# Performance work log

Measured on AMD Instinct MI355X. Metric: run time of the kernel, lower is better.

Reference implementation:

```python
import jax, jax.numpy as jnp
import numpy as np

D_MODEL = 768
D_INNER = 1536   # expand=2
D_STATE = 16
D_CONV = 4
DT_RANK = 48     # ceil(768/16)
B_SZ, L = 2, 2048


def _mamba(h, in_proj, conv_w, conv_b, xproj, dtproj_w, dtproj_b, A_log, Dskip, out_proj):
    """One Mamba block forward. h: [B, L, d_model]."""
    B = h.shape[0]
    xz = h @ in_proj.T                      # [B, L, 2*d_inner]
    x, z = jnp.split(xz, 2, axis=-1)
    # causal depthwise conv over time
    xc = jnp.transpose(x, (0, 2, 1))        # [B, D, L]
    xc = jax.lax.conv_general_dilated(
        xc, conv_w[:, None, :], (1,), [(D_CONV - 1, 0)],
        dimension_numbers=('NCH', 'OIH', 'NCH'), feature_group_count=D_INNER)
    xc = xc + conv_b[None, :, None]
    x = jax.nn.silu(jnp.transpose(xc, (0, 2, 1)))   # [B, L, D]
    # input-dependent dt, B, C
    dbl = x @ xproj.T                                # [B, L, dt_rank + 2*d_state]
    dt, Bm, Cm = jnp.split(dbl, [DT_RANK, DT_RANK + D_STATE], axis=-1)
    dt = jax.nn.softplus(dt @ dtproj_w.T + dtproj_b) # [B, L, D]
    A = -jnp.exp(A_log)                              # [D, N]

    def step(hst, inp):
        x_t, dt_t, B_t, C_t = inp                    # [B,D],[B,D],[B,N],[B,N]
        dA = jnp.exp(dt_t[..., None] * A)            # [B, D, N]
        hst = hst * dA + dt_t[..., None] * B_t[:, None, :] * x_t[..., None]
        y = jnp.einsum('bdn,bn->bd', hst, C_t)
        return hst, y

    h0 = jnp.zeros((B, D_INNER, D_STATE), dtype=h.dtype)
    xs = (jnp.transpose(x, (1, 0, 2)), jnp.transpose(dt, (1, 0, 2)),
          jnp.transpose(Bm, (1, 0, 2)), jnp.transpose(Cm, (1, 0, 2)))
    _, ys = jax.lax.scan(step, h0, xs)               # ys: [L, B, D]
    y = jnp.transpose(ys, (1, 0, 2)) + x * Dskip
    y = y * jax.nn.silu(z)
    return y @ out_proj.T                            # [B, L, d_model]


def _init_params(key):
    ks = jax.random.split(key, 7)
    s = 0.02
    in_proj = jax.random.normal(ks[0], (2 * D_INNER, D_MODEL)) * s
    conv_w = jax.random.normal(ks[1], (D_INNER, D_CONV)) * 0.2
    conv_b = jnp.zeros((D_INNER,))
    xproj = jax.random.normal(ks[2], (DT_RANK + 2 * D_STATE, D_INNER)) * s
    dtproj_w = jax.random.normal(ks[3], (D_INNER, DT_RANK)) * (DT_RANK ** -0.5)
    dtproj_b = jnp.log(jax.random.uniform(ks[4], (D_INNER,), minval=1e-3, maxval=0.1))
    A_log = jnp.log(jnp.tile(jnp.arange(1, D_STATE + 1, dtype=jnp.float32), (D_INNER, 1)))
    Dskip = jnp.ones((D_INNER,))
    out_proj = jax.random.normal(ks[5], (D_MODEL, D_INNER)) * s
    return in_proj, conv_w, conv_b, xproj, dtproj_w, dtproj_b, A_log, Dskip, out_proj


def setup_inputs() -> dict:
    key = jax.random.key(0)
    k_h, k_f, k_r = jax.random.split(key, 3)
    inp = {'hidden_states': jax.random.normal(k_h, (B_SZ, L, D_MODEL), dtype=jnp.float32)}
    names = ['in_proj', 'conv_w', 'conv_b', 'xproj', 'dtproj_w', 'dtproj_b', 'A_log', 'Dskip', 'out_proj']
    for suf, k in (('_f', k_f), ('_r', k_r)):
        for n, p in zip(names, _init_params(k)):
            inp[n + suf] = p
    return inp


def reference(hidden_states,
              in_proj_f, conv_w_f, conv_b_f, xproj_f, dtproj_w_f, dtproj_b_f, A_log_f, Dskip_f, out_proj_f,
              in_proj_r, conv_w_r, conv_b_r, xproj_r, dtproj_w_r, dtproj_b_r, A_log_r, Dskip_r, out_proj_r):
    out = _mamba(hidden_states, in_proj_f, conv_w_f, conv_b_f, xproj_f,
                 dtproj_w_f, dtproj_b_f, A_log_f, Dskip_f, out_proj_f)
    out_rev = _mamba(hidden_states[:, ::-1, :], in_proj_r, conv_w_r, conv_b_r, xproj_r,
                     dtproj_w_r, dtproj_b_r, A_log_r, Dskip_r, out_proj_r)[:, ::-1, :]
    return out + out_rev
```

## Files before the change

kernel.cpp:

```cpp
#include <hip/hip_runtime.h>
#include <hip/hip_bf16.h>
#include <math.h>

#define L_SEQ 2048
#define B_SZ 2
#define D_MODEL 768
#define D_INNER 1536
#define D_STATE 16
#define DT_RANK 48
#define TC 64
#define NC (L_SEQ / TC)
#define NDG (D_INNER / 256)
#define NSPL 4
#define KCH (D_INNER / NSPL)

typedef short bf16x8 __attribute__((ext_vector_type(8)));
typedef float f32x4 __attribute__((ext_vector_type(4)));

#define GLOAD16(g, l) __builtin_amdgcn_global_load_lds( \
    (const __attribute__((address_space(1))) unsigned*)(g), \
    (__attribute__((address_space(3))) unsigned*)(l), 16, 0, 0)

static __device__ __forceinline__ float siluf(float v) {
  return v / (1.0f + __expf(-v));
}
static __device__ __forceinline__ float softplusf(float v) {
  return fmaxf(v, 0.0f) + log1pf(__expf(-fabsf(v)));
}
static __device__ __forceinline__ unsigned short f2bf_rn(float v) {
  unsigned u = __float_as_uint(v);
  u = (u + 0x7fff + ((u >> 16) & 1)) >> 16;
  return (unsigned short)u;
}
static __device__ __forceinline__ float bf2f(unsigned short v) {
  return __uint_as_float((unsigned)v << 16);
}

__global__ __launch_bounds__(256) void cvt_all(
    const float* __restrict__ s_h,  unsigned short* __restrict__ hh,  unsigned short* __restrict__ hl,
    const float* __restrict__ s_w0, unsigned short* __restrict__ w0h, unsigned short* __restrict__ w0l,
    const float* __restrict__ s_w1, unsigned short* __restrict__ w1h, unsigned short* __restrict__ w1l,
    const float* __restrict__ s_o0, unsigned short* __restrict__ o0h, unsigned short* __restrict__ o0l,
    const float* __restrict__ s_o1, unsigned short* __restrict__ o1h, unsigned short* __restrict__ o1l,
    const float* __restrict__ s_x0, unsigned short* __restrict__ x0h, unsigned short* __restrict__ x0l,
    const float* __restrict__ s_x1, unsigned short* __restrict__ x1h, unsigned short* __restrict__ x1l)
{
  long j = (long)blockIdx.x * 256 + threadIdx.x;
  const long N0 = 786432, N1 = 589824, N2 = 589824, N3 = 294912, N4 = 294912, N5 = 30720;
  const float* src; unsigned short *dh, *dl;
  if (j < N0) { src = s_h; dh = hh; dl = hl; }
  else if ((j -= N0) < N1) { src = s_w0; dh = w0h; dl = w0l; }
  else if ((j -= N1) < N2) { src = s_w1; dh = w1h; dl = w1l; }
  else if ((j -= N2) < N3) { src = s_o0; dh = o0h; dl = o0l; }
  else if ((j -= N3) < N4) { src = s_o1; dh = o1h; dl = o1l; }
  else if ((j -= N4) < N5) { src = s_x0; dh = x0h; dl = x0l; }
  else { j -= N5; src = s_x1; dh = x1h; dl = x1l; }
  float4 v = ((const float4*)src)[j];
  float vv[4] = {v.x, v.y, v.z, v.w};
  unsigned short h4[4], l4[4];
  #pragma unroll
  for (int e = 0; e < 4; ++e) {
    unsigned short hv = f2bf_rn(vv[e]);
    h4[e] = hv;
    l4[e] = f2bf_rn(vv[e] - bf2f(hv));
  }
  uint2 ph, pl;
  ph.x = (unsigned)h4[0] | ((unsigned)h4[1] << 16);
  ph.y = (unsigned)h4[2] | ((unsigned)h4[3] << 16);
  pl.x = (unsigned)l4[0] | ((unsigned)l4[1] << 16);
  pl.y = (unsigned)l4[2] | ((unsigned)l4[3] << 16);
  *(uint2*)&dh[j * 4] = ph;
  *(uint2*)&dl[j * 4] = pl;
}

__global__ __launch_bounds__(256) void gemm_inproj(
    const unsigned short* __restrict__ hh, const unsigned short* __restrict__ hl,
    const unsigned short* __restrict__ w0h, const unsigned short* __restrict__ w0l,
    const unsigned short* __restrict__ w1h, const unsigned short* __restrict__ w1l,
    float* __restrict__ xpre, float* __restrict__ zbuf)
{
  __shared__ unsigned short Ah[128 * 32], Al[128 * 32];
  __shared__ unsigned short Wh[128 * 32], Wl[128 * 32];
  const long S1 = (long)B_SZ * L_SEQ * D_INNER;
  const int tid = threadIdx.x;
  const int lane = tid & 63, w = tid >> 6;
  int bid = blockIdx.x;
  int swz = (bid & 7) * 192 + (bid >> 3);
  int dir = swz / 768;
  int rem = swz - dir * 768;
  int mb = rem / 24, nb = rem - (rem / 24) * 24;
  const int m0 = mb * 128, n0 = nb * 128;
  const unsigned short* Whp = dir ? w1h : w0h;
  const unsigned short* Wlp = dir ? w1l : w0l;
  const int ksl = (lane & 3) ^ ((lane >> 3) & 3);
  long aoff[2], woff[2];
  int ldsc[2];
  #pragma unroll
  for (int qq = 0; qq < 2; ++qq) {
    int cq = w * 2 + qq;
    int r = cq * 16 + (lane >> 2);
    int mr = m0 + r;
    int row = dir ? ((mr & ~(L_SEQ - 1)) | ((L_SEQ - 1) - (mr & (L_SEQ - 1)))) : mr;
    aoff[qq] = (long)row * D_MODEL + 8 * ksl;
    woff[qq] = (long)(n0 + r) * D_MODEL + 8 * ksl;
    ldsc[qq] = cq * 512;
  }
  f32x4 acc[4][4];
  #pragma unroll
  for (int i = 0; i < 4; ++i)
    #pragma unroll
    for (int j = 0; j < 4; ++j) acc[i][j] = (f32x4){0.f, 0.f, 0.f, 0.f};
  const int fr = lane & 15, sl = lane >> 4;
  const int wr = w >> 1, wc = w & 1;
  int roffA[4], roffW[4];
  #pragma unroll
  for (int f = 0; f < 4; ++f) {
    int rA = wr * 64 + f * 16 + fr;
    roffA[f] = rA * 32 + ((sl ^ ((rA >> 1) & 3)) * 8);
    int rW = wc * 64 + f * 16 + fr;
    roffW[f] = rW * 32 + ((sl ^ ((rW >> 1) & 3)) * 8);
  }
  for (int k0 = 0; k0 < D_MODEL; k0 += 32) {
    __syncthreads();
    #pragma unroll
    for (int qq = 0; qq < 2; ++qq) {
      GLOAD16(hh + aoff[qq] + k0, &Ah[ldsc[qq]]);
      GLOAD16(hl + aoff[qq] + k0, &Al[ldsc[qq]]);
      GLOAD16(Whp + woff[qq] + k0, &Wh[ldsc[qq]]);
      GLOAD16(Wlp + woff[qq] + k0, &Wl[ldsc[qq]]);
    }
    __syncthreads();
    bf16x8 afh[4], afl[4];
    #pragma unroll
    for (int f = 0; f < 4; ++f) {
      afh[f] = *(const bf16x8*)&Ah[roffA[f]];
      afl[f] = *(const bf16x8*)&Al[roffA[f]];
    }
    #pragma unroll
    for (int fj = 0; fj < 4; ++fj) {
      bf16x8 wfh = *(const bf16x8*)&Wh[roffW[fj]];
      bf16x8 wfl = *(const bf16x8*)&Wl[roffW[fj]];
      #pragma unroll
      for (int fi = 0; fi < 4; ++fi) {
        acc[fi][fj] = __builtin_amdgcn_mfma_f32_16x16x32_bf16(afh[fi], wfh, acc[fi][fj], 0, 0, 0);
        acc[fi][fj] = __builtin_amdgcn_mfma_f32_16x16x32_bf16(afh[fi], wfl, acc[fi][fj], 0, 0, 0);
        acc[fi][fj] = __builtin_amdgcn_mfma_f32_16x16x32_bf16(afl[fi], wfh, acc[fi][fj], 0, 0, 0);
      }
    }
  }
  float* xq = xpre + (long)dir * S1;
  float* zq = zbuf + (long)dir * S1;
  const int fcol = lane & 15, rgrp = lane >> 4;
  #pragma unroll
  for (int fi = 0; fi < 4; ++fi) {
    #pragma unroll
    for (int j = 0; j < 4; ++j) {
      int row = m0 + wr * 64 + fi * 16 + rgrp * 4 + j;
      #pragma unroll
      for (int fj = 0; fj < 4; ++fj) {
        int n = n0 + wc * 64 + fj * 16 + fcol;
        float v = acc[fi][fj][j];
        if (n < D_INNER) xq[(long)row * D_INNER + n] = v;
        else             zq[(long)row * D_INNER + (n - D_INNER)] = v;
      }
    }
  }
}

__global__ __launch_bounds__(256) void xproj_mfma(
    const unsigned short* __restrict__ xh, const unsigned short* __restrict__ xl,
    const unsigned short* __restrict__ x0h, const unsigned short* __restrict__ x0l,
    const unsigned short* __restrict__ x1h, const unsigned short* __restrict__ x1l,
    float* __restrict__ partial)
{
  __shared__ unsigned short Ah[128 * 32], Al[128 * 32];
  __shared__ unsigned short Wh[128 * 32], Wl[128 * 32];
  const long S1 = (long)B_SZ * L_SEQ * D_INNER;
  const int tid = threadIdx.x;
  const int lane = tid & 63, w = tid >> 6;
  int bid = blockIdx.x;
  int dir = bid >> 7;
  int kz = (bid >> 5) & 3;
  int mb = bid & 31;
  const int m0 = mb * 128;
  const int kbase = kz * KCH;
  const unsigned short* Ahp = xh + (long)dir * S1;
  const unsigned short* Alp = xl + (long)dir * S1;
  const unsigned short* Whp = dir ? x1h : x0h;
  const unsigned short* Wlp = dir ? x1l : x0l;
  const int ksl = (lane & 3) ^ ((lane >> 3) & 3);
  long aoff[2], woff[2];
  int ldsc[2], cqv[2];
  #pragma unroll
  for (int qq = 0; qq < 2; ++qq) {
    int cq = w * 2 + qq;
    int r = cq * 16 + (lane >> 2);
    aoff[qq] = (long)(m0 + r) * D_INNER + 8 * ksl + kbase;
    woff[qq] = (long)r * D_INNER + 8 * ksl + kbase;
    ldsc[qq] = cq * 512;
    cqv[qq] = cq;
  }
  for (int i = tid; i < 48 * 32; i += 256) { Wh[80 * 32 + i] = 0; Wl[80 * 32 + i] = 0; }
  f32x4 acc[4][4];
  #pragma unroll
  for (int i = 0; i < 4; ++i)
    #pragma unroll
    for (int j = 0; j < 4; ++j) acc[i][j] = (f32x4){0.f, 0.f, 0.f, 0.f};
  const int fr = lane & 15, sl = lane >> 4;
  const int wr = w >> 1, wc = w & 1;
  int roffA[4], roffW[4];
  #pragma unroll
  for (int f = 0; f < 4; ++f) {
    int rA = wr * 64 + f * 16 + fr;
    roffA[f] = rA * 32 + ((sl ^ ((rA >> 1) & 3)) * 8);
    int rW = wc * 64 + f * 16 + fr;
    roffW[f] = rW * 32 + ((sl ^ ((rW >> 1) & 3)) * 8);
  }
  for (int k0 = 0; k0 < KCH; k0 += 32) {
    __syncthreads();
    #pragma unroll
    for (int qq = 0; qq < 2; ++qq) {
      GLOAD16(Ahp + aoff[qq] + k0, &Ah[ldsc[qq]]);
      GLOAD16(Alp + aoff[qq] + k0, &Al[ldsc[qq]]);
      if (cqv[qq] < 5) {
        GLOAD16(Whp + woff[qq] + k0, &Wh[ldsc[qq]]);
        GLOAD16(Wlp + woff[qq] + k0, &Wl[ldsc[qq]]);
      }
    }
    __syncthreads();
    bf16x8 afh[4], afl[4];
    #pragma unroll
    for (int f = 0; f < 4; ++f) {
      afh[f] = *(const bf16x8*)&Ah[roffA[f]];
      afl[f] = *(const bf16x8*)&Al[roffA[f]];
    }
    #pragma unroll
    for (int fj = 0; fj < 4; ++fj) {
      bf16x8 wfh = *(const bf16x8*)&Wh[roffW[fj]];
      bf16x8 wfl = *(const bf16x8*)&Wl[roffW[fj]];
      #pragma unroll
      for (int fi = 0; fi < 4; ++fi) {
        acc[fi][fj] = __builtin_amdgcn_mfma_f32_16x16x32_bf16(afh[fi], wfh, acc[fi][fj], 0, 0, 0);
        acc[fi][fj] = __builtin_amdgcn_mfma_f32_16x16x32_bf16(afh[fi], wfl, acc[fi][fj], 0, 0, 0);
        acc[fi][fj] = __builtin_amdgcn_mfma_f32_16x16x32_bf16(afl[fi], wfh, acc[fi][fj], 0, 0, 0);
      }
    }
  }
  float* P = partial + (long)(dir * NSPL + kz) * (B_SZ * L_SEQ) * 80;
  const int fcol = lane & 15, rgrp = lane >> 4;
  #pragma unroll
  for (int fi = 0; fi < 4; ++fi) {
    #pragma unroll
    for (int j = 0; j < 4; ++j) {
      int row = m0 + wr * 64 + fi * 16 + rgrp * 4 + j;
      #pragma unroll
      for (int fj = 0; fj < 4; ++fj) {
        int n = wc * 64 + fj * 16 + fcol;
        if (n < 80) P[(long)row * 80 + n] = acc[fi][fj][j];
      }
    }
  }
}

__global__ __launch_bounds__(256) void xproj_reduce(
    const float* __restrict__ partial, float* __restrict__ dbl)
{
  long idx = (long)blockIdx.x * 256 + threadIdx.x;
  const long plane = (long)B_SZ * L_SEQ * 80;
  long dir = idx / plane;
  long rc = idx % plane;
  const float* P = partial + dir * NSPL * plane + rc;
  float s = 0.f;
  #pragma unroll
  for (int z = 0; z < NSPL; ++z) s += P[z * plane];
  dbl[idx] = s;
}

__global__ __launch_bounds__(256) void gemm_outproj_pl(
    const unsigned short* __restrict__ yh, const unsigned short* __restrict__ yl,
    const unsigned short* __restrict__ o0h, const unsigned short* __restrict__ o0l,
    const unsigned short* __restrict__ o1h, const unsigned short* __restrict__ o1l,
    float* __restrict__ partial)
{
  __shared__ unsigned short Ah[128 * 32], Al[128 * 32];
  __shared__ unsigned short Wh[128 * 32], Wl[128 * 32];
  const long S1 = (long)B_SZ * L_SEQ * D_INNER;
  const int tid = threadIdx.x;
  const int lane = tid & 63, w = tid >> 6;
  int bid = blockIdx.x;
  int swz = (bid & 7) * 96 + (bid >> 3);
  int dir = swz / 384;
  int r1 = swz - dir * 384;
  int ks = r1 / 192;
  int r2 = r1 - ks * 192;
  int mb = r2 / 6, nb = r2 - (r2 / 6) * 6;
  const int m0 = mb * 128, n0 = nb * 128;
  const int kbase = ks * (D_INNER / 2);
  const unsigned short* Ahp = yh + (long)dir * S1;
  const unsigned short* Alp = yl + (long)dir * S1;
  const unsigned short* Whp = dir ? o1h : o0h;
  const unsigned short* Wlp = dir ? o1l : o0l;
  const int ksl = (lane & 3) ^ ((lane >> 3) & 3);
  long aoff[2], woff[2];
  int ldsc[2];
  #pragma unroll
  for (int qq = 0; qq < 2; ++qq) {
    int cq = w * 2 + qq;
    int r = cq * 16 + (lane >> 2);
    int mr = m0 + r;
    int row = dir ? ((mr & ~(L_SEQ - 1)) | ((L_SEQ - 1) - (mr & (L_SEQ - 1)))) : mr;
    aoff[qq] = (long)row * D_INNER + 8 * ksl + kbase;
    woff[qq] = (long)(n0 + r) * D_INNER + 8 * ksl + kbase;
    ldsc[qq] = cq * 512;
  }
  f32x4 acc[4][4];
  #pragma unroll
  for (int i = 0; i < 4; ++i)
    #pragma unroll
    for (int j = 0; j < 4; ++j) acc[i][j] = (f32x4){0.f, 0.f, 0.f, 0.f};
  const int fr = lane & 15, sl = lane >> 4;
  const int wr = w >> 1, wc = w & 1;
  int roffA[4], roffW[4];
  #pragma unroll
  for (int f = 0; f < 4; ++f) {
    int rA = wr * 64 + f * 16 + fr;
    roffA[f] = rA * 32 + ((sl ^ ((rA >> 1) & 3)) * 8);
    int rW = wc * 64 + f * 16 + fr;
    roffW[f] = rW * 32 + ((sl ^ ((rW >> 1) & 3)) * 8);
  }
  for (int k0 = 0; k0 < D_INNER / 2; k0 += 32) {
    __syncthreads();
    #pragma unroll
    for (int qq = 0; qq < 2; ++qq) {
      GLOAD16(Ahp + aoff[qq] + k0, &Ah[ldsc[qq]]);
      GLOAD16(Alp + aoff[qq] + k0, &Al[ldsc[qq]]);
      GLOAD16(Whp + woff[qq] + k0, &Wh[ldsc[qq]]);
      GLOAD16(Wlp + woff[qq] + k0, &Wl[ldsc[qq]]);
    }
    __syncthreads();
    bf16x8 afh[4], afl[4];
    #pragma unroll
    for (int f = 0; f < 4; ++f) {
      afh[f] = *(const bf16x8*)&Ah[roffA[f]];
      afl[f] = *(const bf16x8*)&Al[roffA[f]];
    }
    #pragma unroll
    for (int fj = 0; fj < 4; ++fj) {
      bf16x8 wfh = *(const bf16x8*)&Wh[roffW[fj]];
      bf16x8 wfl = *(const bf16x8*)&Wl[roffW[fj]];
      #pragma unroll
      for (int fi = 0; fi < 4; ++fi) {
        acc[fi][fj] = __builtin_amdgcn_mfma_f32_16x16x32_bf16(afh[fi], wfh, acc[fi][fj], 0, 0, 0);
        acc[fi][fj] = __builtin_amdgcn_mfma_f32_16x16x32_bf16(afh[fi], wfl, acc[fi][fj], 0, 0, 0);
        acc[fi][fj] = __builtin_amdgcn_mfma_f32_16x16x32_bf16(afl[fi], wfh, acc[fi][fj], 0, 0, 0);
      }
    }
  }
  float* P = partial + (long)(dir * 2 + ks) * (B_SZ * L_SEQ) * D_MODEL;
  const int fcol = lane & 15, rgrp = lane >> 4;
  #pragma unroll
  for (int fi = 0; fi < 4; ++fi) {
    #pragma unroll
    for (int j = 0; j < 4; ++j) {
      int row = m0 + wr * 64 + fi * 16 + rgrp * 4 + j;
      #pragma unroll
      for (int fj = 0; fj < 4; ++fj) {
        int n = n0 + wc * 64 + fj * 16 + fcol;
        P[(long)row * D_MODEL + n] = acc[fi][fj][j];
      }
    }
  }
}

__global__ __launch_bounds__(256) void outproj_reduce(
    const float* __restrict__ partial, float* __restrict__ out)
{
  long i = (long)blockIdx.x * 256 + threadIdx.x;
  const long plane4 = (long)B_SZ * L_SEQ * D_MODEL / 4;
  float4 a = ((const float4*)partial)[i];
  float4 b = ((const float4*)partial)[i + plane4];
  float4 c = ((const float4*)partial)[i + 2 * plane4];
  float4 d = ((const float4*)partial)[i + 3 * plane4];
  float4 s;
  s.x = (a.x + b.x) + (c.x + d.x);
  s.y = (a.y + b.y) + (c.y + d.y);
  s.z = (a.z + b.z) + (c.z + d.z);
  s.w = (a.w + b.w) + (c.w + d.w);
  ((float4*)out)[i] = s;
}

__global__ __launch_bounds__(256) void conv_silu_pl(
    const float* __restrict__ xpre,
    const float* __restrict__ w_f, const float* __restrict__ b_f,
    const float* __restrict__ w_r, const float* __restrict__ b_r,
    unsigned short* __restrict__ xh, unsigned short* __restrict__ xl)
{
  long i4 = (long)blockIdx.x * 256 + threadIdx.x;
  const long total4 = 2L * B_SZ * L_SEQ * D_INNER / 4;
  if (i4 >= total4) return;
  long idx = i4 * 4;
  int d0 = (int)(idx % D_INNER);
  long r = idx / D_INNER;
  int t = (int)(r & (L_SEQ - 1));
  const float* w  = (r >> 12) ? w_r : w_f;
  const float* cb = (r >> 12) ? b_r : b_f;
  float4 a = *(const float4*)&cb[d0];
  float4 wc[4];
  #pragma unroll
  for (int i = 0; i < 4; ++i) wc[i] = *(const float4*)&w[(d0 + i) * 4];
  #pragma unroll
  for (int k = 0; k < 4; ++k) {
    if (t - 3 + k >= 0) {
      float4 xv = *(const float4*)&xpre[(r - 3 + k) * D_INNER + d0];
      a.x = fmaf(((const float*)&wc[0])[k], xv.x, a.x);
      a.y = fmaf(((const float*)&wc[1])[k], xv.y, a.y);
      a.z = fmaf(((const float*)&wc[2])[k], xv.z, a.z);
      a.w = fmaf(((const float*)&wc[3])[k], xv.w, a.w);
    }
  }
  float vv[4] = {siluf(a.x), siluf(a.y), siluf(a.z), siluf(a.w)};
  unsigned short h4[4], l4[4];
  #pragma unroll
  for (int e = 0; e < 4; ++e) {
    unsigned short hv = f2bf_rn(vv[e]);
    h4[e] = hv;
    l4[e] = f2bf_rn(vv[e] - bf2f(hv));
  }
  uint2 ph, pl;
  ph.x = (unsigned)h4[0] | ((unsigned)h4[1] << 16);
  ph.y = (unsigned)h4[2] | ((unsigned)h4[3] << 16);
  pl.x = (unsigned)l4[0] | ((unsigned)l4[1] << 16);
  pl.y = (unsigned)l4[2] | ((unsigned)l4[3] << 16);
  *(uint2*)&xh[idx] = ph;
  *(uint2*)&xl[idx] = pl;
}

__global__ __launch_bounds__(256) void scan_mega1(
    const unsigned short* __restrict__ xh, const unsigned short* __restrict__ xl,
    const float* __restrict__ dbl,
    const float* __restrict__ dtw_f, const float* __restrict__ dtw_r,
    const float* __restrict__ dtb_f, const float* __restrict__ dtb_r,
    const float* __restrict__ A_log_f, const float* __restrict__ A_log_r,
    float* __restrict__ stateS, float* __restrict__ stateP)
{
  const int tid = threadIdx.x;
  const int chunk = blockIdx.x / NDG;
  const int d = (blockIdx.x % NDG) * 256 + tid;
  const int b = blockIdx.y, dir = blockIdx.z;
  const float* A_log = dir ? A_log_r : A_log_f;
  const float* dtw   = dir ? dtw_r : dtw_f;
  const float dtbv   = (dir ? dtb_r : dtb_f)[d];
  float wreg[48];
  #pragma unroll
  for (int q = 0; q < 12; ++q)
    *(float4*)&wreg[q * 4] = *(const float4*)&dtw[d * DT_RANK + q * 4];
  float Arow[D_STATE];
  #pragma unroll
  for (int n = 0; n < D_STATE; ++n) Arow[n] = -expf(A_log[d * D_STATE + n]);
  float h[D_STATE], P[D_STATE];
  #pragma unroll
  for (int n = 0; n < D_STATE; ++n) { h[n] = 0.f; P[n] = 1.f; }
  const long rowbase = ((long)dir * B_SZ + b) * L_SEQ + (long)chunk * TC;
  for (int tj = 0; tj < TC; ++tj) {
    const float* br = dbl + (rowbase + tj) * 80;
    float dtacc = 0.f;
    #pragma unroll
    for (int q = 0; q < 12; ++q) {
      float4 v = *(const float4*)(br + q * 4);
      dtacc = fmaf(v.x, wreg[q * 4 + 0], dtacc);
      dtacc = fmaf(v.y, wreg[q * 4 + 1], dtacc);
      dtacc = fmaf(v.z, wreg[q * 4 + 2], dtacc);
      dtacc = fmaf(v.w, wreg[q * 4 + 3], dtacc);
    }
    float dtv = softplusf(dtacc + dtbv);
    long off = (rowbase + tj) * D_INNER + d;
    float xv = bf2f(xh[off]) + bf2f(xl[off]);
    float dtx = dtv * xv;
    float bc[D_STATE];
    #pragma unroll
    for (int q = 0; q < 4; ++q)
      *(float4*)&bc[q * 4] = *(const float4*)(br + 48 + q * 4);
    #pragma unroll
    for (int n = 0; n < D_STATE; ++n) {
      float dA = __expf(dtv * Arow[n]);
      P[n] *= dA;
      h[n] = fmaf(h[n], dA, dtx * bc[n]);
    }
  }
  long base = ((((long)dir * B_SZ + b) * NC + chunk) * D_INNER + d) * D_STATE;
  #pragma unroll
  for (int n = 0; n < D_STATE; ++n) { stateS[base + n] = h[n]; stateP[base + n] = P[n]; }
}

__global__ __launch_bounds__(256) void scan_fix(
    float* __restrict__ stateS, const float* __restrict__ stateP)
{
  const long idx = (long)blockIdx.x * 256 + threadIdx.x;
  const int DN = D_INNER * D_STATE;
  const long dirb = idx / DN;
  const int dn = (int)(idx % DN);
  long base = dirb * NC * DN + dn;
  float h = 0.f;
  for (int c = 0; c < NC; ++c) {
    long o = base + (long)c * DN;
    float S = stateS[o];
    float Pc = stateP[o];
    stateS[o] = h;
    h = fmaf(h, Pc, S);
  }
}

__global__ __launch_bounds__(256) void scan_mega2(
    const unsigned short* __restrict__ xh, const unsigned short* __restrict__ xl,
    const float* __restrict__ dbl, const float* __restrict__ z,
    const float* __restrict__ dtw_f, const float* __restrict__ dtw_r,
    const float* __restrict__ dtb_f, const float* __restrict__ dtb_r,
    const float* __restrict__ A_log_f, const float* __restrict__ A_log_r,
    const float* __restrict__ Ds_f, const float* __restrict__ Ds_r,
    const float* __restrict__ stateS,
    unsigned short* __restrict__ yh, unsigned short* __restrict__ yl)
{
  const int tid = threadIdx.x;
  const int chunk = blockIdx.x / NDG;
  const int d = (blockIdx.x % NDG) * 256 + tid;
  const int b = blockIdx.y, dir = blockIdx.z;
  const float* A_log = dir ? A_log_r : A_log_f;
  const float* dtw   = dir ? dtw_r : dtw_f;
  const float dtbv   = (dir ? dtb_r : dtb_f)[d];
  const float Dd     = (dir ? Ds_r : Ds_f)[d];
  float wreg[48];
  #pragma unroll
  for (int q = 0; q < 12; ++q)
    *(float4*)&wreg[q * 4] = *(const float4*)&dtw[d * DT_RANK + q * 4];
  float Arow[D_STATE];
  #pragma unroll
  for (int n = 0; n < D_STATE; ++n) Arow[n] = -expf(A_log[d * D_STATE + n]);
  float h[D_STATE];
  long sbase = ((((long)dir * B_SZ + b) * NC + chunk) * D_INNER + d) * D_STATE;
  #pragma unroll
  for (int n = 0; n < D_STATE; ++n) h[n] = stateS[sbase + n];
  const long rowbase = ((long)dir * B_SZ + b) * L_SEQ + (long)chunk * TC;
  for (int tj = 0; tj < TC; ++tj) {
    const float* br = dbl + (rowbase + tj) * 80;
    float dtacc = 0.f;
    #pragma unroll
    for (int q = 0; q < 12; ++q) {
      float4 v = *(const float4*)(br + q * 4);
      dtacc = fmaf(v.x, wreg[q * 4 + 0], dtacc);
      dtacc = fmaf(v.y, wreg[q * 4 + 1], dtacc);
      dtacc = fmaf(v.z, wreg[q * 4 + 2], dtacc);
      dtacc = fmaf(v.w, wreg[q * 4 + 3], dtacc);
    }
    float dtv = softplusf(dtacc + dtbv);
    long off = (rowbase + tj) * D_INNER + d;
    float xv = bf2f(xh[off]) + bf2f(xl[off]);
    float zv = z[off];
    float dtx = dtv * xv;
    float bc[2 * D_STATE];
    #pragma unroll
    for (int q = 0; q < 8; ++q)
      *(float4*)&bc[q * 4] = *(const float4*)(br + 48 + q * 4);
    float y = 0.f;
    #pragma unroll
    for (int n = 0; n < D_STATE; ++n) {
      float dA = __expf(dtv * Arow[n]);
      h[n] = fmaf(h[n], dA, dtx * bc[n]);
      y = fmaf(h[n], bc[16 + n], y);
    }
    y = fmaf(xv, Dd, y);
    y *= siluf(zv);
    unsigned short hv = f2bf_rn(y);
    yh[off] = hv;
    yl[off] = f2bf_rn(y - bf2f(hv));
  }
}

extern "C" void kernel_launch(void* const* d_in, const int* in_sizes, int n_in,
                              void* d_out, int out_size, void* d_ws, size_t ws_size,
                              hipStream_t stream) {
  const float* h        = (const float*)d_in[0];
  const float* in_proj[2] = {(const float*)d_in[1], (const float*)d_in[10]};
  const float* conv_w[2]  = {(const float*)d_in[2], (const float*)d_in[11]};
  const float* conv_b[2]  = {(const float*)d_in[3], (const float*)d_in[12]};
  const float* xproj[2]   = {(const float*)d_in[4], (const float*)d_in[13]};
  const float* dtw[2]     = {(const float*)d_in[5], (const float*)d_in[14]};
  const float* dtb[2]     = {(const float*)d_in[6], (const float*)d_in[15]};
  const float* A_log[2]   = {(const float*)d_in[7], (const float*)d_in[16]};
  const float* Dsk[2]     = {(const float*)d_in[8], (const float*)d_in[17]};
  const float* outp[2]    = {(const float*)d_in[9], (const float*)d_in[18]};
  float* out = (float*)d_out;
  float* ws = (float*)d_ws;

  const long S1 = (long)B_SZ * L_SEQ * D_INNER;
  const int M = B_SZ * L_SEQ;
  float* xpre  = ws;
  float* zbuf  = ws + 2 * S1;
  float* xconv = ws + 4 * S1;
  float* dbl   = ws + 6 * S1;
  float* base4 = dbl + 2L * M * 80;

  unsigned short* hh  = (unsigned short*)base4;
  unsigned short* hl  = hh + 3145728;
  unsigned short* w0h = hl + 3145728;
  unsigned short* w0l = w0h + 2359296;
  unsigned short* w1h = w0l + 2359296;
  unsigned short* w1l = w1h + 2359296;
  unsigned short* o0h = w1l + 2359296;
  unsigned short* o0l = o0h + 1179648;
  unsigned short* o1h = o0l + 1179648;
  unsigned short* o1l = o1h + 1179648;
  float* xpartial = base4;
  float* stS = base4;
  float* stP = stS + 3145728;
  unsigned short* xw0h = (unsigned short*)dbl;
  unsigned short* xw0l = xw0h + 122880;
  unsigned short* xw1h = xw0l + 122880;
  unsigned short* xw1l = xw1h + 122880;
  unsigned short* xph = (unsigned short*)xconv;
  unsigned short* xpl = xph + 2 * S1;
  unsigned short* yh = (unsigned short*)xpre;
  unsigned short* yl = yh + 2 * S1;
  float* opartial = xconv;

  dim3 blk(256);

  cvt_all<<<dim3(10224), blk, 0, stream>>>(
      h, hh, hl, in_proj[0], w0h, w0l, in_proj[1], w1h, w1l,
      outp[0], o0h, o0l, outp[1], o1h, o1l,
      xproj[0], xw0h, xw0l, xproj[1], xw1h, xw1l);

  gemm_inproj<<<dim3(1536), blk, 0, stream>>>(hh, hl, w0h, w0l, w1h, w1l, xpre, zbuf);

  conv_silu_pl<<<dim3((unsigned)(2 * S1 / 4 / 256)), blk, 0, stream>>>(
      xpre, conv_w[0], conv_b[0], conv_w[1], conv_b[1], xph, xpl);

  xproj_mfma<<<dim3(256), blk, 0, stream>>>(xph, xpl, xw0h, xw0l, xw1h, xw1l, xpartial);
  xproj_reduce<<<dim3((unsigned)(2L * M * 80 / 256)), blk, 0, stream>>>(xpartial, dbl);

  {
    dim3 grid1(NC * NDG, B_SZ, 2);
    scan_mega1<<<grid1, blk, 0, stream>>>(xph, xpl, dbl,
        dtw[0], dtw[1], dtb[0], dtb[1], A_log[0], A_log[1], stS, stP);
    long nfix = 2L * B_SZ * D_INNER * D_STATE;
    scan_fix<<<dim3((unsigned)(nfix / 256)), blk, 0, stream>>>(stS, stP);
    scan_mega2<<<grid1, blk, 0, stream>>>(xph, xpl, dbl, zbuf,
        dtw[0], dtw[1], dtb[0], dtb[1], A_log[0], A_log[1],
        Dsk[0], Dsk[1], stS, yh, yl);
  }
  gemm_outproj_pl<<<dim3(768), blk, 0, stream>>>(yh, yl, o0h, o0l, o1h, o1l, opartial);
  outproj_reduce<<<dim3((unsigned)(M * (long)D_MODEL / 4 / 256)), blk, 0, stream>>>(opartial, out);
}
```

Before: 493.6 us.

## Split dt dot into four accumulators, batch conv over 4 timesteps, prefetch scan_fix loads

The 48-wide dt projection dot product in both scan kernels now uses four independent accumulators, and the time loops are unrolled by 2 to shorten the FMA dependency chain. The depthwise conv kernel has each thread compute four consecutive timesteps from a 7-row window, so the overlapping input rows are read once instead of up to four times. scan_fix loads all chunk states into registers before the sequential combine, which takes the global loads off the serial path. The costs are higher register pressure in the scan kernels and in scan_fix (64 extra floats), and a small change in floating-point summation order.

```diff
diff --git a/kernel.cpp b/kernel.cpp
--- a/kernel.cpp
+++ b/kernel.cpp
@@ -34,6 +34,27 @@
 }
 static __device__ __forceinline__ float bf2f(unsigned short v) {
   return __uint_as_float((unsigned)v << 16);
+}
+static __device__ __forceinline__ float dtdot48(const float* __restrict__ br,
+                                                const float* __restrict__ wreg) {
+  float a0 = 0.f, a1 = 0.f, a2 = 0.f, a3 = 0.f;
+  #pragma unroll
+  for (int q = 0; q < 3; ++q) {
+    float4 v0 = *(const float4*)(br + q * 16 + 0);
+    float4 v1 = *(const float4*)(br + q * 16 + 4);
+    float4 v2 = *(const float4*)(br + q * 16 + 8);
+    float4 v3 = *(const float4*)(br + q * 16 + 12);
+    const float* w = wreg + q * 16;
+    a0 = fmaf(v0.x, w[0], a0);  a0 = fmaf(v0.y, w[1], a0);
+    a0 = fmaf(v0.z, w[2], a0);  a0 = fmaf(v0.w, w[3], a0);
+    a1 = fmaf(v1.x, w[4], a1);  a1 = fmaf(v1.y, w[5], a1);
+    a1 = fmaf(v1.z, w[6], a1);  a1 = fmaf(v1.w, w[7], a1);
+    a2 = fmaf(v2.x, w[8], a2);  a2 = fmaf(v2.y, w[9], a2);
+    a2 = fmaf(v2.z, w[10], a2); a2 = fmaf(v2.w, w[11], a2);
+    a3 = fmaf(v3.x, w[12], a3); a3 = fmaf(v3.y, w[13], a3);
+    a3 = fmaf(v3.z, w[14], a3); a3 = fmaf(v3.w, w[15], a3);
+  }
+  return (a0 + a1) + (a2 + a3);
 }
 
 __global__ __launch_bounds__(256) void cvt_all(
@@ -389,50 +410,63 @@
   ((float4*)out)[i] = s;
 }
 
-__global__ __launch_bounds__(256) void conv_silu_pl(
+__global__ __launch_bounds__(256) void conv_silu_pl4(
     const float* __restrict__ xpre,
     const float* __restrict__ w_f, const float* __restrict__ b_f,
     const float* __restrict__ w_r, const float* __restrict__ b_r,
     unsigned short* __restrict__ xh, unsigned short* __restrict__ xl)
 {
-  long i4 = (long)blockIdx.x * 256 + threadIdx.x;
-  const long total4 = 2L * B_SZ * L_SEQ * D_INNER / 4;
-  if (i4 >= total4) return;
-  long idx = i4 * 4;
-  int d0 = (int)(idx % D_INNER);
-  long r = idx / D_INNER;
-  int t = (int)(r & (L_SEQ - 1));
-  const float* w  = (r >> 12) ? w_r : w_f;
-  const float* cb = (r >> 12) ? b_r : b_f;
-  float4 a = *(const float4*)&cb[d0];
+  long i = (long)blockIdx.x * 256 + threadIdx.x;
+  const int DQ = D_INNER / 4;
+  const long total = 2L * B_SZ * (L_SEQ / 4) * DQ;
+  if (i >= total) return;
+  int dq = (int)(i % DQ);
+  long rq = i / DQ;
+  int t0 = (int)((rq & (L_SEQ / 4 - 1)) * 4);
+  long rbase = (rq >> 9) * L_SEQ;
+  int dir = (int)(rq >> 10);
+  int d0 = dq * 4;
+  const float* w  = dir ? w_r : w_f;
+  const float* cb = dir ? b_r : b_f;
+  float4 bias = *(const float4*)&cb[d0];
   float4 wc[4];
   #pragma unroll
-  for (int i = 0; i < 4; ++i) wc[i] = *(const float4*)&w[(d0 + i) * 4];
-  #pragma unroll
-  for (int k = 0; k < 4; ++k) {
-    if (t - 3 + k >= 0) {
-      float4 xv = *(const float4*)&xpre[(r - 3 + k) * D_INNER + d0];
+  for (int c = 0; c < 4; ++c) wc[c] = *(const float4*)&w[(d0 + c) * 4];
+  float4 xrow[7];
+  #pragma unroll
+  for (int j = 0; j < 7; ++j) {
+    int tv = t0 + j - 3;
+    if (tv >= 0) xrow[j] = *(const float4*)&xpre[(rbase + tv) * D_INNER + d0];
+    else xrow[j] = (float4){0.f, 0.f, 0.f, 0.f};
+  }
+  #pragma unroll
+  for (int u = 0; u < 4; ++u) {
+    float4 a = bias;
+    #pragma unroll
+    for (int k = 0; k < 4; ++k) {
+      float4 xv = xrow[u + k];
       a.x = fmaf(((const float*)&wc[0])[k], xv.x, a.x);
       a.y = fmaf(((const float*)&wc[1])[k], xv.y, a.y);
       a.z = fmaf(((const float*)&wc[2])[k], xv.z, a.z);
       a.w = fmaf(((const float*)&wc[3])[k], xv.w, a.w);
     }
-  }
-  float vv[4] = {siluf(a.x), siluf(a.y), siluf(a.z), siluf(a.w)};
-  unsigned short h4[4], l4[4];
-  #pragma unroll
-  for (int e = 0; e < 4; ++e) {
-    unsigned short hv = f2bf_rn(vv[e]);
-    h4[e] = hv;
-    l4[e] = f2bf_rn(vv[e] - bf2f(hv));
-  }
-  uint2 ph, pl;
-  ph.x = (unsigned)h4[0] | ((unsigned)h4[1] << 16);
-  ph.y = (unsigned)h4[2] | ((unsigned)h4[3] << 16);
-  pl.x = (unsigned)l4[0] | ((unsigned)l4[1] << 16);
-  pl.y = (unsigned)l4[2] | ((unsigned)l4[3] << 16);
-  *(uint2*)&xh[idx] = ph;
-  *(uint2*)&xl[idx] = pl;
+    float vv[4] = {siluf(a.x), siluf(a.y), siluf(a.z), siluf(a.w)};
+    unsigned short h4[4], l4[4];
+    #pragma unroll
+    for (int e = 0; e < 4; ++e) {
+      unsigned short hv = f2bf_rn(vv[e]);
+      h4[e] = hv;
+      l4[e] = f2bf_rn(vv[e] - bf2f(hv));
+    }
+    uint2 ph, pl;
+    ph.x = (unsigned)h4[0] | ((unsigned)h4[1] << 16);
+    ph.y = (unsigned)h4[2] | ((unsigned)h4[3] << 16);
+    pl.x = (unsigned)l4[0] | ((unsigned)l4[1] << 16);
+    pl.y = (unsigned)l4[2] | ((unsigned)l4[3] << 16);
+    long off = (rbase + t0 + u) * D_INNER + d0;
+    *(uint2*)&xh[off] = ph;
+    *(uint2*)&xl[off] = pl;
+  }
 }
 
 __global__ __launch_bounds__(256) void scan_mega1(
@@ -461,18 +495,10 @@
   #pragma unroll
   for (int n = 0; n < D_STATE; ++n) { h[n] = 0.f; P[n] = 1.f; }
   const long rowbase = ((long)dir * B_SZ + b) * L_SEQ + (long)chunk * TC;
+  #pragma unroll 2
   for (int tj = 0; tj < TC; ++tj) {
     const float* br = dbl + (rowbase + tj) * 80;
-    float dtacc = 0.f;
-    #pragma unroll
-    for (int q = 0; q < 12; ++q) {
-      float4 v = *(const float4*)(br + q * 4);
-      dtacc = fmaf(v.x, wreg[q * 4 + 0], dtacc);
-      dtacc = fmaf(v.y, wreg[q * 4 + 1], dtacc);
-      dtacc = fmaf(v.z, wreg[q * 4 + 2], dtacc);
-      dtacc = fmaf(v.w, wreg[q * 4 + 3], dtacc);
-    }
-    float dtv = softplusf(dtacc + dtbv);
+    float dtv = softplusf(dtdot48(br, wreg) + dtbv);
     long off = (rowbase + tj) * D_INNER + d;
     float xv = bf2f(xh[off]) + bf2f(xl[off]);
     float dtx = dtv * xv;
@@ -500,13 +526,17 @@
   const long dirb = idx / DN;
   const int dn = (int)(idx % DN);
   long base = dirb * NC * DN + dn;
+  float S[NC], P[NC];
+  #pragma unroll
+  for (int c = 0; c < NC; ++c) {
+    S[c] = stateS[base + (long)c * DN];
+    P[c] = stateP[base + (long)c * DN];
+  }
   float h = 0.f;
+  #pragma unroll
   for (int c = 0; c < NC; ++c) {
-    long o = base + (long)c * DN;
-    float S = stateS[o];
-    float Pc = stateP[o];
-    stateS[o] = h;
-    h = fmaf(h, Pc, S);
+    stateS[base + (long)c * DN] = h;
+    h = fmaf(h, P[c], S[c]);
   }
 }
 
@@ -540,18 +570,10 @@
   #pragma unroll
   for (int n = 0; n < D_STATE; ++n) h[n] = stateS[sbase + n];
   const long rowbase = ((long)dir * B_SZ + b) * L_SEQ + (long)chunk * TC;
+  #pragma unroll 2
   for (int tj = 0; tj < TC; ++tj) {
     const float* br = dbl + (rowbase + tj) * 80;
-    float dtacc = 0.f;
-    #pragma unroll
-    for (int q = 0; q < 12; ++q) {
-      float4 v = *(const float4*)(br + q * 4);
-      dtacc = fmaf(v.x, wreg[q * 4 + 0], dtacc);
-      dtacc = fmaf(v.y, wreg[q * 4 + 1], dtacc);
-      dtacc = fmaf(v.z, wreg[q * 4 + 2], dtacc);
-      dtacc = fmaf(v.w, wreg[q * 4 + 3], dtacc);
-    }
-    float dtv = softplusf(dtacc + dtbv);
+    float dtv = softplusf(dtdot48(br, wreg) + dtbv);
     long off = (rowbase + tj) * D_INNER + d;
     float xv = bf2f(xh[off]) + bf2f(xl[off]);
     float zv = z[off];
@@ -631,7 +653,7 @@
 
   gemm_inproj<<<dim3(1536), blk, 0, stream>>>(hh, hl, w0h, w0l, w1h, w1l, xpre, zbuf);
 
-  conv_silu_pl<<<dim3((unsigned)(2 * S1 / 4 / 256)), blk, 0, stream>>>(
+  conv_silu_pl4<<<dim3(3072), blk, 0, stream>>>(
       xpre, conv_w[0], conv_b[0], conv_w[1], conv_b[1], xph, xpl);
 
   xproj_mfma<<<dim3(256), blk, 0, stream>>>(xph, xpl, xw0h, xw0l, xw1h, xw1l, xpartial);
```

New measurement: 513.6 us. 4.1% more time.
